# Performance work log

Hardware: AMD Instinct MI355X
Metric: run time of the kernel (lower is better)

The kernel has to match this reference:

```python
import jax, jax.numpy as jnp
import numpy as np

N_NODES = 100000


def gcn_conv(x, edge_index, W, b, n_nodes):
    """PyG GCNConv: linear -> add self-loops -> symmetric-normalized scatter-sum -> bias."""
    h = x @ W  # [N, F_out]
    loop = jnp.arange(n_nodes, dtype=edge_index.dtype)
    src = jnp.concatenate([edge_index[0], loop])
    dst = jnp.concatenate([edge_index[1], loop])
    # degree of destination nodes (self-loops included)
    deg = jax.ops.segment_sum(jnp.ones_like(dst, dtype=h.dtype), dst, num_segments=n_nodes)
    dinv = jnp.where(deg > 0, jax.lax.rsqrt(deg), 0.0)
    norm = dinv[src] * dinv[dst]  # [E+N]
    msg = h[src] * norm[:, None]  # gather + scale
    out = jax.ops.segment_sum(msg, dst, num_segments=n_nodes)  # scatter-add
    return out + b


def setup_inputs() -> dict:
    key = jax.random.key(0)
    k1, k2, k3, k4 = jax.random.split(key, 4)
    d_in, hidden, out = 128, 256, 64
    x = jax.random.normal(k1, (N_NODES, d_in), dtype=jnp.float32)
    edge_index = jax.random.randint(k2, (2, 800000), 0, N_NODES, dtype=jnp.int64)
    W1 = jax.random.normal(k3, (d_in, hidden), dtype=jnp.float32) * (1.0 / np.sqrt(d_in))
    b1 = jnp.zeros((hidden,), dtype=jnp.float32)
    W2 = jax.random.normal(k4, (hidden, out), dtype=jnp.float32) * (1.0 / np.sqrt(hidden))
    b2 = jnp.zeros((out,), dtype=jnp.float32)
    return {"x": x, "edge_index": edge_index, "W1": W1, "b1": b1, "W2": W2, "b2": b2}


def reference(x, edge_index, W1, b1, W2, b2):
    h = jax.nn.relu(gcn_conv(x, edge_index, W1, b1, N_NODES))
    # dropout p=0 (module default) -> identity
    return gcn_conv(h, edge_index, W2, b2, N_NODES)
```

## Files before the change

kernel.cpp:

```cpp
#include <hip/hip_runtime.h>
#include <hip/hip_bf16.h>

#define N_NODES 100000
#define D_IN 128
#define HID 256
#define D_OUT 64
#define TR 32
#define NBUK 196
#define BSH 9
#define MGRID 625

typedef __attribute__((ext_vector_type(8))) short bf8;
typedef __attribute__((ext_vector_type(4))) float f4;

static __device__ __forceinline__ unsigned short f2bf(float f) {
    __hip_bfloat16 h = __float2bfloat16(f);
    return *reinterpret_cast<unsigned short*>(&h);
}
static __device__ __forceinline__ float bflo(unsigned int u) { return __uint_as_float(u << 16); }
static __device__ __forceinline__ float bfhi(unsigned int u) { return __uint_as_float(u & 0xffff0000u); }

static __device__ __forceinline__ void fma8(float* a, float w, uint4 u) {
    a[0] += w * bflo(u.x); a[1] += w * bfhi(u.x);
    a[2] += w * bflo(u.y); a[3] += w * bfhi(u.y);
    a[4] += w * bflo(u.z); a[5] += w * bfhi(u.z);
    a[6] += w * bflo(u.w); a[7] += w * bfhi(u.w);
}
static __device__ __forceinline__ void fma4(float* a, float w, uint2 u) {
    a[0] += w * bflo(u.x); a[1] += w * bfhi(u.x);
    a[2] += w * bflo(u.y); a[3] += w * bfhi(u.y);
}


__global__ __launch_bounds__(256) void k_prep(const float* __restrict__ x,
                                              unsigned long long* __restrict__ xb,
                                              const float* __restrict__ W1,
                                              unsigned short* __restrict__ W1t,
                                              const float* __restrict__ W2,
                                              unsigned short* __restrict__ W2t,
                                              const int* __restrict__ dst, int E,
                                              int* __restrict__ hist2d) {
    int b = blockIdx.x, t = threadIdx.x;
    if (b < 12500) {
        int i = b * 256 + t;
        float4 v = ((const float4*)x)[i];
        unsigned long long o = (unsigned long long)f2bf(v.x) |
                               ((unsigned long long)f2bf(v.y) << 16) |
                               ((unsigned long long)f2bf(v.z) << 32) |
                               ((unsigned long long)f2bf(v.w) << 48);
        xb[i] = o;
    } else if (b < 12628) {
        int i = (b - 12500) * 256 + t;
        int n = i >> 7, k = i & 127;
        W1t[i] = f2bf(W1[k * HID + n]);
    } else if (b < 12692) {
        int i = (b - 12628) * 256 + t;
        int n = i >> 8, k = i & 255;
        W2t[i] = f2bf(W2[k * D_OUT + n]);
    } else {
        int hb = b - 12692;
        __shared__ int h[NBUK];
        if (t < NBUK) h[t] = 0;
        __syncthreads();
        int base = hb * 4096;
        for (int j = 0; j < 16; j++) {
            int e = base + j * 256 + t;
            if (e < E) atomicAdd(&h[dst[e] >> BSH], 1);
        }
        __syncthreads();
        if (t < NBUK) hist2d[hb * NBUK + t] = h[t];
    }
}


__global__ __launch_bounds__(256) void k_scanB1(const int* __restrict__ hist2d,
                                                int* __restrict__ blockbase,
                                                int* __restrict__ bsumB, int nbb) {
    __shared__ int s[256];
    int u = blockIdx.x, t = threadIdx.x;
    int v = (t < nbb) ? hist2d[t * NBUK + u] : 0;
    s[t] = v;
    __syncthreads();
    for (int off = 1; off < 256; off <<= 1) {
        int w = (t >= off) ? s[t - off] : 0;
        __syncthreads();
        s[t] += w;
        __syncthreads();
    }
    if (t < nbb) blockbase[t * NBUK + u] = s[t] - v;
    if (t == 255) bsumB[u] = s[255];
}


__global__ __launch_bounds__(256) void k_scanB2(const int* __restrict__ bsumB,
                                                int* __restrict__ bbase) {
    __shared__ int s[256];
    int t = threadIdx.x;
    int v = (t < NBUK) ? bsumB[t] : 0;
    s[t] = v;
    __syncthreads();
    for (int off = 1; off < 256; off <<= 1) {
        int w = (t >= off) ? s[t - off] : 0;
        __syncthreads();
        s[t] += w;
        __syncthreads();
    }
    if (t < NBUK) bbase[t] = s[t] - v;
    if (t == NBUK - 1) bbase[NBUK] = s[t];
}


__global__ __launch_bounds__(256) void k_bin(const int* __restrict__ src,
                                             const int* __restrict__ dst, int E,
                                             const int* __restrict__ blockbase,
                                             const int* __restrict__ bbase,
                                             unsigned int* __restrict__ bin) {
    __shared__ int baseL[NBUK], rankL[NBUK];
    int t = threadIdx.x;
    if (t < NBUK) {
        baseL[t] = bbase[t] + blockbase[blockIdx.x * NBUK + t];
        rankL[t] = 0;
    }
    __syncthreads();
    int base = blockIdx.x * 4096;
    for (int j = 0; j < 16; j++) {
        int e = base + j * 256 + t;
        if (e < E) {
            int s = src[e], d = dst[e];
            int bu = d >> BSH;
            int r = atomicAdd(&rankL[bu], 1);
            bin[baseL[bu] + r] = ((unsigned int)(d & 511) << 17) | (unsigned int)s;
        }
    }
}


__global__ __launch_bounds__(256) void k_cntscan(const unsigned int* __restrict__ bin,
                                                 const int* __restrict__ bbase,
                                                 int* __restrict__ row_ptr,
                                                 int* __restrict__ bsum,
                                                 float* __restrict__ dinv) {
    __shared__ int c[512];
    __shared__ int s[256];
    int b = blockIdx.x, t = threadIdx.x;
    c[t] = 0;
    c[t + 256] = 0;
    __syncthreads();
    int lo = bbase[b], hi = bbase[b + 1];
    for (int e = lo + t; e < hi; e += 256) atomicAdd(&c[bin[e] >> 17], 1);
    __syncthreads();
    int a0 = c[2 * t], a1 = c[2 * t + 1];
    s[t] = a0 + a1;
    __syncthreads();
    for (int off = 1; off < 256; off <<= 1) {
        int u = (t >= off) ? s[t - off] : 0;
        __syncthreads();
        s[t] += u;
        __syncthreads();
    }
    int ex = (t > 0) ? s[t - 1] : 0;
    int n0 = (b << BSH) + 2 * t;
    if (n0 < N_NODES) {
        row_ptr[n0] = ex;
        dinv[n0] = rsqrtf((float)a0 + 1.0f);
    }
    if (n0 + 1 < N_NODES) {
        row_ptr[n0 + 1] = ex + a0;
        dinv[n0 + 1] = rsqrtf((float)a1 + 1.0f);
    }
    if (t == 255) bsum[b] = s[255];
}


__global__ __launch_bounds__(256) void k_place(const unsigned int* __restrict__ bin,
                                               const int* __restrict__ bbase,
                                               const int* __restrict__ bsum,
                                               int* __restrict__ row_ptr,
                                               const float* __restrict__ dinv,
                                               int2* __restrict__ cw) {
    __shared__ int sc[256];
    __shared__ int cur[512];
    __shared__ float dl[512];
    int b = blockIdx.x, t = threadIdx.x;
    sc[t] = (t < NBUK) ? bsum[t] : 0;
    __syncthreads();
    for (int off = 1; off < 256; off <<= 1) {
        int u = (t >= off) ? sc[t - off] : 0;
        __syncthreads();
        sc[t] += u;
        __syncthreads();
    }
    int base = (b > 0) ? sc[b - 1] : 0;
    if (b == NBUK - 1 && t == 0) row_ptr[N_NODES] = sc[NBUK - 1];
    int node0 = b << BSH;
    int nbn = N_NODES - node0;
    if (nbn > 512) nbn = 512;
    if (t < nbn) {
        int v = row_ptr[node0 + t] + base;
        cur[t] = v;
        row_ptr[node0 + t] = v;
        dl[t] = dinv[node0 + t];
    }
    if (t + 256 < nbn) {
        int v = row_ptr[node0 + t + 256] + base;
        cur[t + 256] = v;
        row_ptr[node0 + t + 256] = v;
        dl[t + 256] = dinv[node0 + t + 256];
    }
    __syncthreads();
    int lo = bbase[b], hi = bbase[b + 1];
    for (int e = lo + t; e < hi; e += 256) {
        unsigned int rec = bin[e];
        int s = rec & 0x1FFFF;
        int dloc = rec >> 17;
        int pos = atomicAdd(&cur[dloc], 1);
        int2 v;
        v.x = s;
        v.y = __float_as_int(dinv[s] * dl[dloc]);
        cw[pos] = v;
    }
}


__global__ __launch_bounds__(256) void k_pull1(const int* __restrict__ row_ptr,
                                               const int2* __restrict__ cw,
                                               const uint4* __restrict__ xb4,
                                               const float* __restrict__ dinv,
                                               uint4* __restrict__ agg4) {
    int wave = (blockIdx.x * 256 + threadIdx.x) >> 6;
    int lane = threadIdx.x & 63;
    int g = lane >> 4, l = lane & 15;
    int node = wave * 4 + g;
    int beg = row_ptr[node], end = row_ptr[node + 1];
    float di = dinv[node];
    float a[8] = {0, 0, 0, 0, 0, 0, 0, 0};
    fma8(a, di * di, xb4[(size_t)node * 16 + l]);
    int e = beg;
    if (e + 4 <= end) {
        int2 c0 = cw[e], c1 = cw[e + 1], c2 = cw[e + 2], c3 = cw[e + 3];
        uint4 u0 = xb4[(size_t)c0.x * 16 + l];
        uint4 u1 = xb4[(size_t)c1.x * 16 + l];
        uint4 u2 = xb4[(size_t)c2.x * 16 + l];
        uint4 u3 = xb4[(size_t)c3.x * 16 + l];
        e += 4;
        for (; e + 4 <= end; e += 4) {
            int2 d0 = cw[e], d1 = cw[e + 1], d2 = cw[e + 2], d3 = cw[e + 3];
            uint4 v0 = xb4[(size_t)d0.x * 16 + l];
            uint4 v1 = xb4[(size_t)d1.x * 16 + l];
            uint4 v2 = xb4[(size_t)d2.x * 16 + l];
            uint4 v3 = xb4[(size_t)d3.x * 16 + l];
            fma8(a, __int_as_float(c0.y), u0);
            fma8(a, __int_as_float(c1.y), u1);
            fma8(a, __int_as_float(c2.y), u2);
            fma8(a, __int_as_float(c3.y), u3);
            c0 = d0; c1 = d1; c2 = d2; c3 = d3;
            u0 = v0; u1 = v1; u2 = v2; u3 = v3;
        }
        fma8(a, __int_as_float(c0.y), u0);
        fma8(a, __int_as_float(c1.y), u1);
        fma8(a, __int_as_float(c2.y), u2);
        fma8(a, __int_as_float(c3.y), u3);
    }
    for (; e < end; e++) {
        int2 c = cw[e];
        fma8(a, __int_as_float(c.y), xb4[(size_t)c.x * 16 + l]);
    }
    uint4 o;
    o.x = (unsigned int)f2bf(a[0]) | ((unsigned int)f2bf(a[1]) << 16);
    o.y = (unsigned int)f2bf(a[2]) | ((unsigned int)f2bf(a[3]) << 16);
    o.z = (unsigned int)f2bf(a[4]) | ((unsigned int)f2bf(a[5]) << 16);
    o.w = (unsigned int)f2bf(a[6]) | ((unsigned int)f2bf(a[7]) << 16);
    agg4[(size_t)node * 16 + l] = o;
}


__global__ __launch_bounds__(256) void k_fused_mfma(unsigned short* __restrict__ agg,
                                                    const unsigned short* __restrict__ W1t,
                                                    const float* __restrict__ b1,
                                                    const unsigned short* __restrict__ W2t) {
    __shared__ char sH[TR * HID * 2];
    int t = threadIdx.x, wave = t >> 6, lane = t & 63;
    int lr = lane & 15, lg = lane >> 4;

    bf8 w1f[4][4];
#pragma unroll
    for (int kk = 0; kk < 4; kk++)
#pragma unroll
        for (int tt = 0; tt < 4; tt++)
            w1f[kk][tt] = *(const bf8*)(W1t + (size_t)(wave * 64 + tt * 16 + lr) * D_IN + kk * 32 + lg * 8);
    bf8 w2f[8];
#pragma unroll
    for (int kk = 0; kk < 8; kk++)
        w2f[kk] = *(const bf8*)(W2t + (size_t)(wave * 16 + lr) * HID + kk * 32 + lg * 8);
    float bias[4];
#pragma unroll
    for (int tt = 0; tt < 4; tt++) bias[tt] = b1[wave * 64 + tt * 16 + lr];

    for (int it = 0; it < 5; it++) {
        size_t row0 = ((size_t)blockIdx.x + (size_t)it * MGRID) * TR;

        f4 acc1[4][2];
#pragma unroll
        for (int tt = 0; tt < 4; tt++)
#pragma unroll
            for (int h = 0; h < 2; h++) acc1[tt][h] = (f4){0.f, 0.f, 0.f, 0.f};

#pragma unroll
        for (int kk = 0; kk < 4; kk++) {
            bf8 a0 = *(const bf8*)(agg + (row0 + lr) * 128 + kk * 32 + lg * 8);
            bf8 a1 = *(const bf8*)(agg + (row0 + 16 + lr) * 128 + kk * 32 + lg * 8);
#pragma unroll
            for (int tt = 0; tt < 4; tt++) {
                acc1[tt][0] = __builtin_amdgcn_mfma_f32_16x16x32_bf16(a0, w1f[kk][tt], acc1[tt][0], 0, 0, 0);
                acc1[tt][1] = __builtin_amdgcn_mfma_f32_16x16x32_bf16(a1, w1f[kk][tt], acc1[tt][1], 0, 0, 0);
            }
        }

#pragma unroll
        for (int tt = 0; tt < 4; tt++) {
            int colc = wave * 64 + tt * 16 + lr;
#pragma unroll
            for (int h = 0; h < 2; h++) {
#pragma unroll
                for (int ri = 0; ri < 4; ri++) {
                    int row = h * 16 + lg * 4 + ri;
                    float hv = acc1[tt][h][ri] + bias[tt];
                    hv = hv > 0.f ? hv : 0.f;
                    *(unsigned short*)(sH + ((row * 512 + colc * 2) ^ ((row & 7) << 4))) = f2bf(hv);
                }
            }
        }
        __syncthreads();

        f4 acc2[2];
        acc2[0] = (f4){0.f, 0.f, 0.f, 0.f};
        acc2[1] = (f4){0.f, 0.f, 0.f, 0.f};
#pragma unroll
        for (int kk = 0; kk < 8; kk++) {
            bf8 a0 = *(const bf8*)(sH + ((lr * 512 + kk * 64 + lg * 16) ^ ((lr & 7) << 4)));
            bf8 a1 = *(const bf8*)(sH + (((16 + lr) * 512 + kk * 64 + lg * 16) ^ (((16 + lr) & 7) << 4)));
            acc2[0] = __builtin_amdgcn_mfma_f32_16x16x32_bf16(a0, w2f[kk], acc2[0], 0, 0, 0);
            acc2[1] = __builtin_amdgcn_mfma_f32_16x16x32_bf16(a1, w2f[kk], acc2[1], 0, 0, 0);
        }
        int colc = wave * 16 + lr;
#pragma unroll
        for (int h = 0; h < 2; h++)
#pragma unroll
            for (int ri = 0; ri < 4; ri++) {
                int row = h * 16 + lg * 4 + ri;
                agg[(row0 + row) * 128 + colc] = f2bf(acc2[h][ri]);
            }
        __syncthreads();
    }
}


__global__ __launch_bounds__(256) void k_pull2(const int* __restrict__ row_ptr,
                                               const int2* __restrict__ cw,
                                               const uint2* __restrict__ m2,
                                               const float* __restrict__ dinv,
                                               const float* __restrict__ b2,
                                               float4* __restrict__ out4) {
    int wave = (blockIdx.x * 256 + threadIdx.x) >> 6;
    int lane = threadIdx.x & 63;
    int g = lane >> 4, l = lane & 15;
    int node = wave * 4 + g;
    int beg = row_ptr[node], end = row_ptr[node + 1];
    float di = dinv[node];
    float a[4] = {0, 0, 0, 0};
    fma4(a, di * di, m2[(size_t)node * 32 + l]);
    int e = beg;
    if (e + 4 <= end) {
        int2 c0 = cw[e], c1 = cw[e + 1], c2 = cw[e + 2], c3 = cw[e + 3];
        uint2 u0 = m2[(size_t)c0.x * 32 + l];
        uint2 u1 = m2[(size_t)c1.x * 32 + l];
        uint2 u2 = m2[(size_t)c2.x * 32 + l];
        uint2 u3 = m2[(size_t)c3.x * 32 + l];
        e += 4;
        for (; e + 4 <= end; e += 4) {
            int2 d0 = cw[e], d1 = cw[e + 1], d2 = cw[e + 2], d3 = cw[e + 3];
            uint2 v0 = m2[(size_t)d0.x * 32 + l];
            uint2 v1 = m2[(size_t)d1.x * 32 + l];
            uint2 v2 = m2[(size_t)d2.x * 32 + l];
            uint2 v3 = m2[(size_t)d3.x * 32 + l];
            fma4(a, __int_as_float(c0.y), u0);
            fma4(a, __int_as_float(c1.y), u1);
            fma4(a, __int_as_float(c2.y), u2);
            fma4(a, __int_as_float(c3.y), u3);
            c0 = d0; c1 = d1; c2 = d2; c3 = d3;
            u0 = v0; u1 = v1; u2 = v2; u3 = v3;
        }
        fma4(a, __int_as_float(c0.y), u0);
        fma4(a, __int_as_float(c1.y), u1);
        fma4(a, __int_as_float(c2.y), u2);
        fma4(a, __int_as_float(c3.y), u3);
    }
    for (; e < end; e++) {
        int2 c = cw[e];
        fma4(a, __int_as_float(c.y), m2[(size_t)c.x * 32 + l]);
    }
    float4 bv = ((const float4*)b2)[l];
    float4 o;
    o.x = a[0] + bv.x;
    o.y = a[1] + bv.y;
    o.z = a[2] + bv.z;
    o.w = a[3] + bv.w;
    out4[(size_t)node * 16 + l] = o;
}


extern "C" void kernel_launch(void* const* d_in, const int* in_sizes, int n_in,
                              void* d_out, int out_size, void* d_ws, size_t ws_size,
                              hipStream_t stream) {
    const float* x  = (const float*)d_in[0];
    const int*   ei = (const int*)d_in[1];
    const float* W1 = (const float*)d_in[2];
    const float* b1 = (const float*)d_in[3];
    const float* W2 = (const float*)d_in[4];
    const float* b2 = (const float*)d_in[5];
    float* out = (float*)d_out;

    const int E = in_sizes[1] / 2;
    const int* src = ei;
    const int* dst = ei + E;

    char* ws = (char*)d_ws;
    int* row_ptr        = (int*)(ws + 0);
    int2* cw            = (int2*)(ws + 400640);
    float* dinv         = (float*)(ws + 6800640);
    unsigned short* W1t = (unsigned short*)(ws + 7201024);
    unsigned short* W2t = (unsigned short*)(ws + 7266560);
    unsigned short* xb  = (unsigned short*)(ws + 7299328);
    unsigned short* aggb = (unsigned short*)(ws + 32899328);
    unsigned int* bin   = (unsigned int*)aggb;
    int* hist2d         = (int*)((char*)aggb + 3200256);
    int* blockbase      = (int*)((char*)aggb + 3354112);
    int* bbase          = (int*)((char*)aggb + 3507968);
    int* bsum           = (int*)((char*)aggb + 3509248);
    int* bsumB          = (int*)((char*)aggb + 3510272);

    const int NBB = (E + 4095) / 4096;

    k_prep<<<12692 + NBB, 256, 0, stream>>>(x, (unsigned long long*)xb, W1, W1t, W2, W2t,
                                            dst, E, hist2d);
    k_scanB1<<<NBUK, 256, 0, stream>>>(hist2d, blockbase, bsumB, NBB);
    k_scanB2<<<1, 256, 0, stream>>>(bsumB, bbase);
    k_bin<<<NBB, 256, 0, stream>>>(src, dst, E, blockbase, bbase, bin);
    k_cntscan<<<NBUK, 256, 0, stream>>>(bin, bbase, row_ptr, bsum, dinv);
    k_place<<<NBUK, 256, 0, stream>>>(bin, bbase, bsum, row_ptr, dinv, cw);
    k_pull1<<<6250, 256, 0, stream>>>(row_ptr, cw, (const uint4*)xb, dinv, (uint4*)aggb);
    k_fused_mfma<<<MGRID, 256, 0, stream>>>(aggb, W1t, b1, W2t);
    k_pull2<<<6250, 256, 0, stream>>>(row_ptr, cw, (const uint2*)aggb, dinv, b2, (float4*)out);
}
```

Measured before the change: 150.3 us.

## Fuse layer-1 aggregation with both MFMA matmuls and fold bucket scan into consumers

Layer-1 neighbour aggregation is merged with the two dense MFMA matmuls into one kernel. Each block gathers 32 rows into swizzled LDS, then runs the W1+bias+ReLU and W2 products from shared memory, and writes a compact 64-wide bf16 message buffer. This removes the global round trip of the aggregated features and one launch. The single-block bucket scan kernel is also dropped: each consumer block recomputes the small scan redundantly, and row_ptr gets its global offsets directly in k_cntscan. In exchange, W1/W2 fragments are reloaded by every one of 3125 blocks, and the fused kernel's gather phase may suffer lower occupancy from the larger LDS footprint.

Measured after the change: 154.2 us. +2.6%, slower.

```diff
diff --git a/kernel.cpp b/kernel.cpp
--- a/kernel.cpp
+++ b/kernel.cpp
@@ -8,7 +8,6 @@
 #define TR 32
 #define NBUK 196
 #define BSH 9
-#define MGRID 625
 
 typedef __attribute__((ext_vector_type(8))) short bf8;
 typedef __attribute__((ext_vector_type(4))) float f4;
@@ -91,11 +90,8 @@
     if (t == 255) bsumB[u] = s[255];
 }
 
-
-__global__ __launch_bounds__(256) void k_scanB2(const int* __restrict__ bsumB,
-                                                int* __restrict__ bbase) {
-    __shared__ int s[256];
-    int t = threadIdx.x;
+static __device__ __forceinline__ void bucket_scan(const int* __restrict__ bsumB,
+                                                   int* s, int* exs, int t) {
     int v = (t < NBUK) ? bsumB[t] : 0;
     s[t] = v;
     __syncthreads();
@@ -105,20 +101,23 @@
         s[t] += w;
         __syncthreads();
     }
-    if (t < NBUK) bbase[t] = s[t] - v;
-    if (t == NBUK - 1) bbase[NBUK] = s[t];
+    if (t < NBUK) exs[t] = s[t] - v;
+    if (t == NBUK - 1) exs[NBUK] = s[t];
+    __syncthreads();
 }
 
 
 __global__ __launch_bounds__(256) void k_bin(const int* __restrict__ src,
                                              const int* __restrict__ dst, int E,
                                              const int* __restrict__ blockbase,
-                                             const int* __restrict__ bbase,
+                                             const int* __restrict__ bsumB,
                                              unsigned int* __restrict__ bin) {
+    __shared__ int s[256], exs[NBUK + 1];
     __shared__ int baseL[NBUK], rankL[NBUK];
     int t = threadIdx.x;
+    bucket_scan(bsumB, s, exs, t);
     if (t < NBUK) {
-        baseL[t] = bbase[t] + blockbase[blockIdx.x * NBUK + t];
+        baseL[t] = exs[t] + blockbase[blockIdx.x * NBUK + t];
         rankL[t] = 0;
     }
     __syncthreads();
@@ -126,27 +125,28 @@
     for (int j = 0; j < 16; j++) {
         int e = base + j * 256 + t;
         if (e < E) {
-            int s = src[e], d = dst[e];
+            int sv = src[e], d = dst[e];
             int bu = d >> BSH;
             int r = atomicAdd(&rankL[bu], 1);
-            bin[baseL[bu] + r] = ((unsigned int)(d & 511) << 17) | (unsigned int)s;
+            bin[baseL[bu] + r] = ((unsigned int)(d & 511) << 17) | (unsigned int)sv;
         }
     }
 }
 
 
 __global__ __launch_bounds__(256) void k_cntscan(const unsigned int* __restrict__ bin,
-                                                 const int* __restrict__ bbase,
+                                                 const int* __restrict__ bsumB,
                                                  int* __restrict__ row_ptr,
-                                                 int* __restrict__ bsum,
                                                  float* __restrict__ dinv) {
+    __shared__ int sb[256], exs[NBUK + 1];
     __shared__ int c[512];
     __shared__ int s[256];
     int b = blockIdx.x, t = threadIdx.x;
+    bucket_scan(bsumB, sb, exs, t);
+    int lo = exs[b], hi = exs[b + 1];
     c[t] = 0;
     c[t + 256] = 0;
     __syncthreads();
-    int lo = bbase[b], hi = bbase[b + 1];
     for (int e = lo + t; e < hi; e += 256) atomicAdd(&c[bin[e] >> 17], 1);
     __syncthreads();
     int a0 = c[2 * t], a1 = c[2 * t + 1];
@@ -161,197 +161,178 @@
     int ex = (t > 0) ? s[t - 1] : 0;
     int n0 = (b << BSH) + 2 * t;
     if (n0 < N_NODES) {
-        row_ptr[n0] = ex;
+        row_ptr[n0] = lo + ex;
         dinv[n0] = rsqrtf((float)a0 + 1.0f);
     }
     if (n0 + 1 < N_NODES) {
-        row_ptr[n0 + 1] = ex + a0;
+        row_ptr[n0 + 1] = lo + ex + a0;
         dinv[n0 + 1] = rsqrtf((float)a1 + 1.0f);
     }
-    if (t == 255) bsum[b] = s[255];
+    if (b == NBUK - 1 && t == 255) row_ptr[N_NODES] = exs[NBUK];
 }
 
 
 __global__ __launch_bounds__(256) void k_place(const unsigned int* __restrict__ bin,
-                                               const int* __restrict__ bbase,
-                                               const int* __restrict__ bsum,
-                                               int* __restrict__ row_ptr,
+                                               const int* __restrict__ bsumB,
+                                               const int* __restrict__ row_ptr,
                                                const float* __restrict__ dinv,
                                                int2* __restrict__ cw) {
-    __shared__ int sc[256];
+    __shared__ int sb[256], exs[NBUK + 1];
     __shared__ int cur[512];
     __shared__ float dl[512];
     int b = blockIdx.x, t = threadIdx.x;
-    sc[t] = (t < NBUK) ? bsum[t] : 0;
-    __syncthreads();
-    for (int off = 1; off < 256; off <<= 1) {
-        int u = (t >= off) ? sc[t - off] : 0;
-        __syncthreads();
-        sc[t] += u;
-        __syncthreads();
-    }
-    int base = (b > 0) ? sc[b - 1] : 0;
-    if (b == NBUK - 1 && t == 0) row_ptr[N_NODES] = sc[NBUK - 1];
+    bucket_scan(bsumB, sb, exs, t);
     int node0 = b << BSH;
     int nbn = N_NODES - node0;
     if (nbn > 512) nbn = 512;
     if (t < nbn) {
-        int v = row_ptr[node0 + t] + base;
-        cur[t] = v;
-        row_ptr[node0 + t] = v;
+        cur[t] = row_ptr[node0 + t];
         dl[t] = dinv[node0 + t];
     }
     if (t + 256 < nbn) {
-        int v = row_ptr[node0 + t + 256] + base;
-        cur[t + 256] = v;
-        row_ptr[node0 + t + 256] = v;
+        cur[t + 256] = row_ptr[node0 + t + 256];
         dl[t + 256] = dinv[node0 + t + 256];
     }
     __syncthreads();
-    int lo = bbase[b], hi = bbase[b + 1];
+    int lo = exs[b], hi = exs[b + 1];
     for (int e = lo + t; e < hi; e += 256) {
         unsigned int rec = bin[e];
-        int s = rec & 0x1FFFF;
+        int sv = rec & 0x1FFFF;
         int dloc = rec >> 17;
         int pos = atomicAdd(&cur[dloc], 1);
         int2 v;
-        v.x = s;
-        v.y = __float_as_int(dinv[s] * dl[dloc]);
+        v.x = sv;
+        v.y = __float_as_int(dinv[sv] * dl[dloc]);
         cw[pos] = v;
     }
 }
 
 
-__global__ __launch_bounds__(256) void k_pull1(const int* __restrict__ row_ptr,
-                                               const int2* __restrict__ cw,
-                                               const uint4* __restrict__ xb4,
-                                               const float* __restrict__ dinv,
-                                               uint4* __restrict__ agg4) {
-    int wave = (blockIdx.x * 256 + threadIdx.x) >> 6;
-    int lane = threadIdx.x & 63;
+__global__ __launch_bounds__(256) void k_pull1m(const int* __restrict__ row_ptr,
+                                                const int2* __restrict__ cw,
+                                                const uint4* __restrict__ xb4,
+                                                const float* __restrict__ dinv,
+                                                const unsigned short* __restrict__ W1t,
+                                                const float* __restrict__ b1,
+                                                const unsigned short* __restrict__ W2t,
+                                                unsigned short* __restrict__ mb) {
+    __shared__ char sA[TR * 256];
+    __shared__ char sH[TR * 512];
+    int t = threadIdx.x, wave = t >> 6, lane = t & 63;
     int g = lane >> 4, l = lane & 15;
-    int node = wave * 4 + g;
-    int beg = row_ptr[node], end = row_ptr[node + 1];
-    float di = dinv[node];
-    float a[8] = {0, 0, 0, 0, 0, 0, 0, 0};
-    fma8(a, di * di, xb4[(size_t)node * 16 + l]);
-    int e = beg;
-    if (e + 4 <= end) {
-        int2 c0 = cw[e], c1 = cw[e + 1], c2 = cw[e + 2], c3 = cw[e + 3];
-        uint4 u0 = xb4[(size_t)c0.x * 16 + l];
-        uint4 u1 = xb4[(size_t)c1.x * 16 + l];
-        uint4 u2 = xb4[(size_t)c2.x * 16 + l];
-        uint4 u3 = xb4[(size_t)c3.x * 16 + l];
-        e += 4;
-        for (; e + 4 <= end; e += 4) {
-            int2 d0 = cw[e], d1 = cw[e + 1], d2 = cw[e + 2], d3 = cw[e + 3];
-            uint4 v0 = xb4[(size_t)d0.x * 16 + l];
-            uint4 v1 = xb4[(size_t)d1.x * 16 + l];
-            uint4 v2 = xb4[(size_t)d2.x * 16 + l];
-            uint4 v3 = xb4[(size_t)d3.x * 16 + l];
+    size_t row0 = (size_t)blockIdx.x * TR;
+
+    for (int r = 0; r < 2; r++) {
+        int row = r * 16 + wave * 4 + g;
+        int node = (int)row0 + row;
+        int beg = row_ptr[node], end = row_ptr[node + 1];
+        float di = dinv[node];
+        float a[8] = {0, 0, 0, 0, 0, 0, 0, 0};
+        fma8(a, di * di, xb4[(size_t)node * 16 + l]);
+        int e = beg;
+        if (e + 4 <= end) {
+            int2 c0 = cw[e], c1 = cw[e + 1], c2 = cw[e + 2], c3 = cw[e + 3];
+            uint4 u0 = xb4[(size_t)c0.x * 16 + l];
+            uint4 u1 = xb4[(size_t)c1.x * 16 + l];
+            uint4 u2 = xb4[(size_t)c2.x * 16 + l];
+            uint4 u3 = xb4[(size_t)c3.x * 16 + l];
+            e += 4;
+            for (; e + 4 <= end; e += 4) {
+                int2 d0 = cw[e], d1 = cw[e + 1], d2 = cw[e + 2], d3 = cw[e + 3];
+                uint4 v0 = xb4[(size_t)d0.x * 16 + l];
+                uint4 v1 = xb4[(size_t)d1.x * 16 + l];
+                uint4 v2 = xb4[(size_t)d2.x * 16 + l];
+                uint4 v3 = xb4[(size_t)d3.x * 16 + l];
+                fma8(a, __int_as_float(c0.y), u0);
+                fma8(a, __int_as_float(c1.y), u1);
+                fma8(a, __int_as_float(c2.y), u2);
+                fma8(a, __int_as_float(c3.y), u3);
+                c0 = d0; c1 = d1; c2 = d2; c3 = d3;
+                u0 = v0; u1 = v1; u2 = v2; u3 = v3;
+            }
             fma8(a, __int_as_float(c0.y), u0);
             fma8(a, __int_as_float(c1.y), u1);
             fma8(a, __int_as_float(c2.y), u2);
             fma8(a, __int_as_float(c3.y), u3);
-            c0 = d0; c1 = d1; c2 = d2; c3 = d3;
-            u0 = v0; u1 = v1; u2 = v2; u3 = v3;
-        }
-        fma8(a, __int_as_float(c0.y), u0);
-        fma8(a, __int_as_float(c1.y), u1);
-        fma8(a, __int_as_float(c2.y), u2);
-        fma8(a, __int_as_float(c3.y), u3);
-    }
-    for (; e < end; e++) {
-        int2 c = cw[e];
-        fma8(a, __int_as_float(c.y), xb4[(size_t)c.x * 16 + l]);
-    }
-    uint4 o;
-    o.x = (unsigned int)f2bf(a[0]) | ((unsigned int)f2bf(a[1]) << 16);
-    o.y = (unsigned int)f2bf(a[2]) | ((unsigned int)f2bf(a[3]) << 16);
-    o.z = (unsigned int)f2bf(a[4]) | ((unsigned int)f2bf(a[5]) << 16);
-    o.w = (unsigned int)f2bf(a[6]) | ((unsigned int)f2bf(a[7]) << 16);
-    agg4[(size_t)node * 16 + l] = o;
-}
-
-
-__global__ __launch_bounds__(256) void k_fused_mfma(unsigned short* __restrict__ agg,
-                                                    const unsigned short* __restrict__ W1t,
-                                                    const float* __restrict__ b1,
-                                                    const unsigned short* __restrict__ W2t) {
-    __shared__ char sH[TR * HID * 2];
-    int t = threadIdx.x, wave = t >> 6, lane = t & 63;
+        }
+        for (; e < end; e++) {
+            int2 c = cw[e];
+            fma8(a, __int_as_float(c.y), xb4[(size_t)c.x * 16 + l]);
+        }
+        uint4 o;
+        o.x = (unsigned int)f2bf(a[0]) | ((unsigned int)f2bf(a[1]) << 16);
+        o.y = (unsigned int)f2bf(a[2]) | ((unsigned int)f2bf(a[3]) << 16);
+        o.z = (unsigned int)f2bf(a[4]) | ((unsigned int)f2bf(a[5]) << 16);
+        o.w = (unsigned int)f2bf(a[6]) | ((unsigned int)f2bf(a[7]) << 16);
+        *(uint4*)(sA + ((row * 256 + l * 16) ^ ((row & 7) << 4))) = o;
+    }
+    __syncthreads();
+
     int lr = lane & 15, lg = lane >> 4;
-
-    bf8 w1f[4][4];
-#pragma unroll
-    for (int kk = 0; kk < 4; kk++)
-#pragma unroll
-        for (int tt = 0; tt < 4; tt++)
-            w1f[kk][tt] = *(const bf8*)(W1t + (size_t)(wave * 64 + tt * 16 + lr) * D_IN + kk * 32 + lg * 8);
-    bf8 w2f[8];
-#pragma unroll
-    for (int kk = 0; kk < 8; kk++)
-        w2f[kk] = *(const bf8*)(W2t + (size_t)(wave * 16 + lr) * HID + kk * 32 + lg * 8);
-    float bias[4];
-#pragma unroll
-    for (int tt = 0; tt < 4; tt++) bias[tt] = b1[wave * 64 + tt * 16 + lr];
-
-    for (int it = 0; it < 5; it++) {
-        size_t row0 = ((size_t)blockIdx.x + (size_t)it * MGRID) * TR;
-
-        f4 acc1[4][2];
-#pragma unroll
-        for (int tt = 0; tt < 4; tt++)
-#pragma unroll
-            for (int h = 0; h < 2; h++) acc1[tt][h] = (f4){0.f, 0.f, 0.f, 0.f};
-
+#pragma unroll
+    for (int th = 0; th < 2; th++) {
+        bf8 w1f[4][2];
+#pragma unroll
+        for (int kk = 0; kk < 4; kk++)
+#pragma unroll
+            for (int q = 0; q < 2; q++)
+                w1f[kk][q] = *(const bf8*)(W1t + (size_t)(wave * 64 + (th * 2 + q) * 16 + lr) * D_IN + kk * 32 + lg * 8);
+        f4 acc[2][2];
+#pragma unroll
+        for (int q = 0; q < 2; q++) {
+            acc[q][0] = (f4){0.f, 0.f, 0.f, 0.f};
+            acc[q][1] = (f4){0.f, 0.f, 0.f, 0.f};
+        }
 #pragma unroll
         for (int kk = 0; kk < 4; kk++) {
-            bf8 a0 = *(const bf8*)(agg + (row0 + lr) * 128 + kk * 32 + lg * 8);
-            bf8 a1 = *(const bf8*)(agg + (row0 + 16 + lr) * 128 + kk * 32 + lg * 8);
-#pragma unroll
-            for (int tt = 0; tt < 4; tt++) {
-                acc1[tt][0] = __builtin_amdgcn_mfma_f32_16x16x32_bf16(a0, w1f[kk][tt], acc1[tt][0], 0, 0, 0);
-                acc1[tt][1] = __builtin_amdgcn_mfma_f32_16x16x32_bf16(a1, w1f[kk][tt], acc1[tt][1], 0, 0, 0);
+            bf8 a0 = *(const bf8*)(sA + ((lr * 256 + kk * 64 + lg * 16) ^ ((lr & 7) << 4)));
+            bf8 a1 = *(const bf8*)(sA + (((16 + lr) * 256 + kk * 64 + lg * 16) ^ (((16 + lr) & 7) << 4)));
+#pragma unroll
+            for (int q = 0; q < 2; q++) {
+                acc[q][0] = __builtin_amdgcn_mfma_f32_16x16x32_bf16(a0, w1f[kk][q], acc[q][0], 0, 0, 0);
+                acc[q][1] = __builtin_amdgcn_mfma_f32_16x16x32_bf16(a1, w1f[kk][q], acc[q][1], 0, 0, 0);
             }
         }
-
-#pragma unroll
-        for (int tt = 0; tt < 4; tt++) {
-            int colc = wave * 64 + tt * 16 + lr;
+#pragma unroll
+        for (int q = 0; q < 2; q++) {
+            int colc = wave * 64 + (th * 2 + q) * 16 + lr;
+            float bias = b1[colc];
 #pragma unroll
             for (int h = 0; h < 2; h++) {
 #pragma unroll
                 for (int ri = 0; ri < 4; ri++) {
                     int row = h * 16 + lg * 4 + ri;
-                    float hv = acc1[tt][h][ri] + bias[tt];
+                    float hv = acc[q][h][ri] + bias;
                     hv = hv > 0.f ? hv : 0.f;
                     *(unsigned short*)(sH + ((row * 512 + colc * 2) ^ ((row & 7) << 4))) = f2bf(hv);
                 }
             }
         }
-        __syncthreads();
-
-        f4 acc2[2];
-        acc2[0] = (f4){0.f, 0.f, 0.f, 0.f};
-        acc2[1] = (f4){0.f, 0.f, 0.f, 0.f};
-#pragma unroll
-        for (int kk = 0; kk < 8; kk++) {
-            bf8 a0 = *(const bf8*)(sH + ((lr * 512 + kk * 64 + lg * 16) ^ ((lr & 7) << 4)));
-            bf8 a1 = *(const bf8*)(sH + (((16 + lr) * 512 + kk * 64 + lg * 16) ^ (((16 + lr) & 7) << 4)));
-            acc2[0] = __builtin_amdgcn_mfma_f32_16x16x32_bf16(a0, w2f[kk], acc2[0], 0, 0, 0);
-            acc2[1] = __builtin_amdgcn_mfma_f32_16x16x32_bf16(a1, w2f[kk], acc2[1], 0, 0, 0);
-        }
-        int colc = wave * 16 + lr;
-#pragma unroll
-        for (int h = 0; h < 2; h++)
-#pragma unroll
-            for (int ri = 0; ri < 4; ri++) {
-                int row = h * 16 + lg * 4 + ri;
-                agg[(row0 + row) * 128 + colc] = f2bf(acc2[h][ri]);
-            }
-        __syncthreads();
-    }
+    }
+    __syncthreads();
+
+    bf8 w2f[8];
+#pragma unroll
+    for (int kk = 0; kk < 8; kk++)
+        w2f[kk] = *(const bf8*)(W2t + (size_t)(wave * 16 + lr) * HID + kk * 32 + lg * 8);
+    f4 acc2[2];
+    acc2[0] = (f4){0.f, 0.f, 0.f, 0.f};
+    acc2[1] = (f4){0.f, 0.f, 0.f, 0.f};
+#pragma unroll
+    for (int kk = 0; kk < 8; kk++) {
+        bf8 a0 = *(const bf8*)(sH + ((lr * 512 + kk * 64 + lg * 16) ^ ((lr & 7) << 4)));
+        bf8 a1 = *(const bf8*)(sH + (((16 + lr) * 512 + kk * 64 + lg * 16) ^ (((16 + lr) & 7) << 4)));
+        acc2[0] = __builtin_amdgcn_mfma_f32_16x16x32_bf16(a0, w2f[kk], acc2[0], 0, 0, 0);
+        acc2[1] = __builtin_amdgcn_mfma_f32_16x16x32_bf16(a1, w2f[kk], acc2[1], 0, 0, 0);
+    }
+    int colc = wave * 16 + lr;
+#pragma unroll
+    for (int h = 0; h < 2; h++)
+#pragma unroll
+        for (int ri = 0; ri < 4; ri++) {
+            int row = h * 16 + lg * 4 + ri;
+            mb[(row0 + row) * D_OUT + colc] = f2bf(acc2[h][ri]);
+        }
 }
 
 
@@ -368,21 +349,21 @@
     int beg = row_ptr[node], end = row_ptr[node + 1];
     float di = dinv[node];
     float a[4] = {0, 0, 0, 0};
-    fma4(a, di * di, m2[(size_t)node * 32 + l]);
+    fma4(a, di * di, m2[(size_t)node * 16 + l]);
     int e = beg;
     if (e + 4 <= end) {
         int2 c0 = cw[e], c1 = cw[e + 1], c2 = cw[e + 2], c3 = cw[e + 3];
-        uint2 u0 = m2[(size_t)c0.x * 32 + l];
-        uint2 u1 = m2[(size_t)c1.x * 32 + l];
-        uint2 u2 = m2[(size_t)c2.x * 32 + l];
-        uint2 u3 = m2[(size_t)c3.x * 32 + l];
+        uint2 u0 = m2[(size_t)c0.x * 16 + l];
+        uint2 u1 = m2[(size_t)c1.x * 16 + l];
+        uint2 u2 = m2[(size_t)c2.x * 16 + l];
+        uint2 u3 = m2[(size_t)c3.x * 16 + l];
         e += 4;
         for (; e + 4 <= end; e += 4) {
             int2 d0 = cw[e], d1 = cw[e + 1], d2 = cw[e + 2], d3 = cw[e + 3];
-            uint2 v0 = m2[(size_t)d0.x * 32 + l];
-            uint2 v1 = m2[(size_t)d1.x * 32 + l];
-            uint2 v2 = m2[(size_t)d2.x * 32 + l];
-            uint2 v3 = m2[(size_t)d3.x * 32 + l];
+            uint2 v0 = m2[(size_t)d0.x * 16 + l];
+            uint2 v1 = m2[(size_t)d1.x * 16 + l];
+            uint2 v2 = m2[(size_t)d2.x * 16 + l];
+            uint2 v3 = m2[(size_t)d3.x * 16 + l];
             fma4(a, __int_as_float(c0.y), u0);
             fma4(a, __int_as_float(c1.y), u1);
             fma4(a, __int_as_float(c2.y), u2);
@@ -397,7 +378,7 @@
     }
     for (; e < end; e++) {
         int2 c = cw[e];
-        fma4(a, __int_as_float(c.y), m2[(size_t)c.x * 32 + l]);
+        fma4(a, __int_as_float(c.y), m2[(size_t)c.x * 16 + l]);
     }
     float4 bv = ((const float4*)b2)[l];
     float4 o;
@@ -431,24 +412,20 @@
     unsigned short* W1t = (unsigned short*)(ws + 7201024);
     unsigned short* W2t = (unsigned short*)(ws + 7266560);
     unsigned short* xb  = (unsigned short*)(ws + 7299328);
-    unsigned short* aggb = (unsigned short*)(ws + 32899328);
-    unsigned int* bin   = (unsigned int*)aggb;
-    int* hist2d         = (int*)((char*)aggb + 3200256);
-    int* blockbase      = (int*)((char*)aggb + 3354112);
-    int* bbase          = (int*)((char*)aggb + 3507968);
-    int* bsum           = (int*)((char*)aggb + 3509248);
-    int* bsumB          = (int*)((char*)aggb + 3510272);
+    unsigned short* mb  = (unsigned short*)(ws + 32899328);
+    unsigned int* bin   = (unsigned int*)mb;
+    int* hist2d         = (int*)((char*)mb + 3200256);
+    int* blockbase      = (int*)((char*)mb + 3354112);
+    int* bsumB          = (int*)((char*)mb + 3507968);
 
     const int NBB = (E + 4095) / 4096;
 
     k_prep<<<12692 + NBB, 256, 0, stream>>>(x, (unsigned long long*)xb, W1, W1t, W2, W2t,
                                             dst, E, hist2d);
     k_scanB1<<<NBUK, 256, 0, stream>>>(hist2d, blockbase, bsumB, NBB);
-    k_scanB2<<<1, 256, 0, stream>>>(bsumB, bbase);
-    k_bin<<<NBB, 256, 0, stream>>>(src, dst, E, blockbase, bbase, bin);
-    k_cntscan<<<NBUK, 256, 0, stream>>>(bin, bbase, row_ptr, bsum, dinv);
-    k_place<<<NBUK, 256, 0, stream>>>(bin, bbase, bsum, row_ptr, dinv, cw);
-    k_pull1<<<6250, 256, 0, stream>>>(row_ptr, cw, (const uint4*)xb, dinv, (uint4*)aggb);
-    k_fused_mfma<<<MGRID, 256, 0, stream>>>(aggb, W1t, b1, W2t);
-    k_pull2<<<6250, 256, 0, stream>>>(row_ptr, cw, (const uint2*)aggb, dinv, b2, (float4*)out);
-}
+    k_bin<<<NBB, 256, 0, stream>>>(src, dst, E, blockbase, bsumB, bin);
+    k_cntscan<<<NBUK, 256, 0, stream>>>(bin, bsumB, row_ptr, dinv);
+    k_place<<<NBUK, 256, 0, stream>>>(bin, bsumB, row_ptr, dinv, cw);
+    k_pull1m<<<3125, 256, 0, stream>>>(row_ptr, cw, (const uint4*)xb, dinv, W1t, b1, W2t, mb);
+    k_pull2<<<6250, 256, 0, stream>>>(row_ptr, cw, (const uint2*)mb, dinv, b2, (float4*)out);
+}
```
